# Optimization experiments

Hardware: AMD Instinct MI355X
Metric: run time of the kernel (lower is better)

The kernel has to match this reference:

```python
import jax, jax.numpy as jnp
import numpy as np

H, RANK, BATCH, T = 1024, 4, 128, 256


def setup_inputs() -> dict:
    key = jax.random.key(0)
    ks = jax.random.split(key, 6)
    s = 1.0 / np.sqrt(H)  # glorot-ish scale for params
    return {
        "x": jax.random.normal(ks[0], (BATCH, T, H), jnp.float32),
        "h0": jnp.zeros((BATCH, H), jnp.float32),
        "d": jax.random.normal(ks[1], (H,), jnp.float32) * s,
        "L": jax.random.normal(ks[2], (H, RANK), jnp.float32) * s,
        "R": jax.random.normal(ks[3], (RANK, H), jnp.float32) * s,
        "B": jax.random.normal(ks[4], (H, H), jnp.float32) * s,
    }


def reference(x, h0, d, L, R, B):
    # Input projection B.T @ x_t for all steps at once (one big GEMM):
    # (B.T @ x)_i = sum_j B[j,i] x[j]  ->  x @ B
    xB = jnp.einsum("bth,hk->btk", x, B)  # [batch, T, H]

    def step(h, u):  # h: [batch, H], u: [batch, H]
        # diagonal + rank-4 low-rank update: d*h + L @ (R @ h) + B.T @ x
        low_rank = (h @ R.T) @ L.T  # [batch, H]
        h = jnp.tanh(d * h + low_rank + u)
        return h, h

    _, hs = jax.lax.scan(step, h0, jnp.swapaxes(xB, 0, 1))  # hs: [T, batch, H]
    return jnp.swapaxes(hs, 0, 1)  # [batch, T, H]
```

## Files before the change

### kernel.cpp

```cpp
#include <hip/hip_runtime.h>
#include <hip/hip_bf16.h>

#define H_DIM  1024
#define RANK_  4
#define BATCH_ 128
#define TSTEPS 256
#define M_DIM  (BATCH_ * TSTEPS)

typedef __bf16 bf16x8 __attribute__((ext_vector_type(8)));
typedef float  floatx4 __attribute__((ext_vector_type(4)));
typedef unsigned short ushortx8 __attribute__((ext_vector_type(8)));

__device__ __forceinline__ unsigned short f2bf(float f) {
    unsigned u = __float_as_uint(f);
    u += 0x7FFFu + ((u >> 16) & 1u);
    return (unsigned short)(u >> 16);
}


__global__ __launch_bounds__(256) void cvt_x_kernel(const float* __restrict__ x,
                                                    unsigned short* __restrict__ xb) {
    size_t i = ((size_t)blockIdx.x * 256 + threadIdx.x) * 8;
    float4 v0 = *(const float4*)(x + i);
    float4 v1 = *(const float4*)(x + i + 4);
    ushortx8 o;
    o[0] = f2bf(v0.x); o[1] = f2bf(v0.y); o[2] = f2bf(v0.z); o[3] = f2bf(v0.w);
    o[4] = f2bf(v1.x); o[5] = f2bf(v1.y); o[6] = f2bf(v1.z); o[7] = f2bf(v1.w);
    *(ushortx8*)(xb + i) = o;
}

__global__ __launch_bounds__(256) void cvt_bt_kernel(const float* __restrict__ B,
                                                     unsigned short* __restrict__ Bt) {
    __shared__ float tl[32][33];
    int tx = threadIdx.x & 31, ty = threadIdx.x >> 5;
    int k0 = blockIdx.y * 32, n0 = blockIdx.x * 32;
#pragma unroll
    for (int j = 0; j < 4; ++j)
        tl[ty + 8 * j][tx] = B[(size_t)(k0 + ty + 8 * j) * H_DIM + n0 + tx];
    __syncthreads();
#pragma unroll
    for (int j = 0; j < 4; ++j)
        Bt[(size_t)(n0 + ty + 8 * j) * H_DIM + k0 + tx] = f2bf(tl[tx][ty + 8 * j]);
}


#define TM 128
#define TN 128
#define BK 64

__global__ __launch_bounds__(256) void gemm_bf16_kernel(const unsigned short* __restrict__ A,
                                                        const unsigned short* __restrict__ Bt,
                                                        float* __restrict__ C) {
    __shared__ unsigned short As[TM * BK];
    __shared__ unsigned short Bs[TN * BK];

    const int tid  = threadIdx.x;
    const int lane = tid & 63;
    const int wid  = tid >> 6;
    const int wm = (wid >> 1) * 64, wn = (wid & 1) * 64;
    const int bm = blockIdx.x >> 3, bn = blockIdx.x & 7;
    const int m0 = bm * TM, n0 = bn * TN;

    const int lr = lane & 15;
    const int lk = (lane >> 4) * 8;

    const unsigned short* ag[4];
    const unsigned short* bg[4];
    unsigned short* asl[4];
    unsigned short* bsl[4];
#pragma unroll
    for (int p = 0; p < 4; ++p) {
        const int ab = wid * 4 + p;
        const int rb = ab >> 1, kb = ab & 1;
        ag[p]  = A  + (size_t)(m0 + rb * 16 + lr) * H_DIM + kb * 32 + lk;
        bg[p]  = Bt + (size_t)(n0 + rb * 16 + lr) * H_DIM + kb * 32 + lk;
        asl[p] = As + ab * 512;
        bsl[p] = Bs + ab * 512;
    }

    floatx4 acc[4][4];
#pragma unroll
    for (int i = 0; i < 4; ++i)
#pragma unroll
        for (int j = 0; j < 4; ++j) acc[i][j] = (floatx4){0.f, 0.f, 0.f, 0.f};

    for (int kt = 0; kt < H_DIM; kt += BK) {
        __syncthreads();
#pragma unroll
        for (int p = 0; p < 4; ++p) {
            __builtin_amdgcn_global_load_lds(
                (const __attribute__((address_space(1))) void*)(ag[p] + kt),
                (__attribute__((address_space(3))) void*)asl[p], 16, 0, 0);
            __builtin_amdgcn_global_load_lds(
                (const __attribute__((address_space(1))) void*)(bg[p] + kt),
                (__attribute__((address_space(3))) void*)bsl[p], 16, 0, 0);
        }
        __syncthreads();
#pragma unroll
        for (int kb = 0; kb < 2; ++kb) {
            bf16x8 af[4], bfv[4];
#pragma unroll
            for (int i = 0; i < 4; ++i) {
                const int rbA = (wm >> 4) + i;
                af[i] = *(const bf16x8*)(As + ((rbA * 2 + kb) << 9) + (lane << 3));
            }
#pragma unroll
            for (int j = 0; j < 4; ++j) {
                const int rbB = (wn >> 4) + j;
                bfv[j] = *(const bf16x8*)(Bs + ((rbB * 2 + kb) << 9) + (lane << 3));
            }
#pragma unroll
            for (int i = 0; i < 4; ++i)
#pragma unroll
                for (int j = 0; j < 4; ++j)
                    acc[i][j] = __builtin_amdgcn_mfma_f32_16x16x32_bf16(af[i], bfv[j], acc[i][j], 0, 0, 0);
        }
    }

    const int cr = (lane >> 4) * 4;
    const int cc = lane & 15;
#pragma unroll
    for (int i = 0; i < 4; ++i)
#pragma unroll
        for (int j = 0; j < 4; ++j) {
            size_t base = (size_t)(m0 + wm + i * 16 + cr) * H_DIM + (n0 + wn + j * 16 + cc);
#pragma unroll
            for (int r = 0; r < 4; ++r)
                C[base + (size_t)r * H_DIM] = acc[i][j][r];
        }
}

__global__ __launch_bounds__(256) void gemm_fp32_fallback(const float* __restrict__ A,
                                                          const float* __restrict__ B,
                                                          float* __restrict__ C) {
    __shared__ float As[64][20];
    __shared__ float Bs[16][68];
    const int tid = threadIdx.x;
    const int bm = blockIdx.x >> 4, bn = blockIdx.x & 15;
    const int m0 = bm * 64, n0 = bn * 64;
    const int tx = (tid & 15) * 4, ty = (tid >> 4) * 4;
    float acc[4][4];
#pragma unroll
    for (int i = 0; i < 4; ++i)
#pragma unroll
        for (int j = 0; j < 4; ++j) acc[i][j] = 0.f;

    for (int kk = 0; kk < H_DIM; kk += 16) {
        float4 av = *(const float4*)(A + (size_t)(m0 + (tid >> 2)) * H_DIM + kk + (tid & 3) * 4);
        float4 bv = *(const float4*)(B + (size_t)(kk + (tid >> 4)) * H_DIM + n0 + (tid & 15) * 4);
        __syncthreads();
        *(float4*)&As[tid >> 2][(tid & 3) * 4] = av;
        *(float4*)&Bs[tid >> 4][(tid & 15) * 4] = bv;
        __syncthreads();
#pragma unroll
        for (int k = 0; k < 16; ++k) {
            float a_[4], b_[4];
#pragma unroll
            for (int i = 0; i < 4; ++i) a_[i] = As[ty + i][k];
#pragma unroll
            for (int j = 0; j < 4; ++j) b_[j] = Bs[k][tx + j];
#pragma unroll
            for (int i = 0; i < 4; ++i)
#pragma unroll
                for (int j = 0; j < 4; ++j) acc[i][j] += a_[i] * b_[j];
        }
    }
#pragma unroll
    for (int i = 0; i < 4; ++i)
#pragma unroll
        for (int j = 0; j < 4; ++j)
            C[(size_t)(m0 + ty + i) * H_DIM + n0 + tx + j] = acc[i][j];
}


__device__ __forceinline__ float tanh_fast(float x) {
    float ax = fabsf(x);
    float e  = __expf(-2.0f * ax);
    float t  = (1.0f - e) * __builtin_amdgcn_rcpf(1.0f + e);
    return copysignf(t, x);
}

__device__ __forceinline__ void barrier_lds_only() {
    asm volatile("s_waitcnt lgkmcnt(0)\n\ts_barrier" ::: "memory");
}

template <int CTRL, int RMASK>
__device__ __forceinline__ float dpp_add(float x) {
    int v = __builtin_amdgcn_update_dpp(0, __float_as_int(x), CTRL, RMASK, 0xf, true);
    return x + __int_as_float(v);
}
__device__ __forceinline__ float wave_sum64(float x) {
    x = dpp_add<0x111, 0xf>(x);
    x = dpp_add<0x112, 0xf>(x);
    x = dpp_add<0x114, 0xf>(x);
    x = dpp_add<0x118, 0xf>(x);
    x = dpp_add<0x142, 0xa>(x);
    x = dpp_add<0x143, 0xc>(x);
    return x;
}

__global__ __launch_bounds__(256) void scan_kernel(const float* __restrict__ h0,
                                                   const float* __restrict__ d,
                                                   const float* __restrict__ Lm,
                                                   const float* __restrict__ Rm,
                                                   float* __restrict__ io) {
    const int b = blockIdx.x, tid = threadIdx.x;
    const int lane = tid & 63, wv = tid >> 6;
    const int e = tid * 4;

    float4 dv4 = *(const float4*)(d + e);
    float dd[4] = {dv4.x, dv4.y, dv4.z, dv4.w};
    float4 hv4 = *(const float4*)(h0 + (size_t)b * H_DIM + e);
    float h[4] = {hv4.x, hv4.y, hv4.z, hv4.w};

    float Lv[4][4], Rv[4][4];
#pragma unroll
    for (int i = 0; i < 4; ++i) {
        float4 t = *(const float4*)(Lm + (size_t)(e + i) * RANK_);
        Lv[i][0] = t.x; Lv[i][1] = t.y; Lv[i][2] = t.z; Lv[i][3] = t.w;
    }
#pragma unroll
    for (int j = 0; j < 4; ++j) {
        float4 t = *(const float4*)(Rm + (size_t)j * H_DIM + e);
        Rv[j][0] = t.x; Rv[j][1] = t.y; Rv[j][2] = t.z; Rv[j][3] = t.w;
    }

    float* iob = io + (size_t)b * TSTEPS * H_DIM + e;
    __shared__ float red[2][4][4];

    float4 u[4];
#pragma unroll
    for (int s = 0; s < 4; ++s) u[s] = *(const float4*)(iob + (size_t)s * H_DIM);

    for (int t = 0; t < TSTEPS; t += 4) {
#pragma unroll
        for (int s = 0; s < 4; ++s) {
            const int tt = t + s;
            float pr[4];
#pragma unroll
            for (int j = 0; j < 4; ++j)
                pr[j] = Rv[j][0] * h[0] + Rv[j][1] * h[1] + Rv[j][2] * h[2] + Rv[j][3] * h[3];
#pragma unroll
            for (int j = 0; j < 4; ++j) pr[j] = wave_sum64(pr[j]);
            if (lane == 63) {
                float4 w; w.x = pr[0]; w.y = pr[1]; w.z = pr[2]; w.w = pr[3];
                *(float4*)&red[s & 1][wv][0] = w;
            }
            barrier_lds_only();
            float4 r0 = *(const float4*)&red[s & 1][0][0];
            float4 r1 = *(const float4*)&red[s & 1][1][0];
            float4 r2 = *(const float4*)&red[s & 1][2][0];
            float4 r3 = *(const float4*)&red[s & 1][3][0];
            float r[4] = {r0.x + r1.x + r2.x + r3.x, r0.y + r1.y + r2.y + r3.y,
                          r0.z + r1.z + r2.z + r3.z, r0.w + r1.w + r2.w + r3.w};

            float uu[4] = {u[s].x, u[s].y, u[s].z, u[s].w};
#pragma unroll
            for (int i = 0; i < 4; ++i) {
                float a = fmaf(dd[i], h[i], uu[i]);
                a += Lv[i][0] * r[0] + Lv[i][1] * r[1] + Lv[i][2] * r[2] + Lv[i][3] * r[3];
                h[i] = tanh_fast(a);
            }
            float4 o; o.x = h[0]; o.y = h[1]; o.z = h[2]; o.w = h[3];
            *(float4*)(iob + (size_t)tt * H_DIM) = o;
            if (tt + 4 < TSTEPS) u[s] = *(const float4*)(iob + (size_t)(tt + 4) * H_DIM);
        }
    }
}


extern "C" void kernel_launch(void* const* d_in, const int* in_sizes, int n_in,
                              void* d_out, int out_size, void* d_ws, size_t ws_size,
                              hipStream_t stream) {
    const float* x  = (const float*)d_in[0];
    const float* h0 = (const float*)d_in[1];
    const float* dd = (const float*)d_in[2];
    const float* L  = (const float*)d_in[3];
    const float* R  = (const float*)d_in[4];
    const float* B  = (const float*)d_in[5];
    float* out = (float*)d_out;

    const size_t need = (size_t)M_DIM * H_DIM * sizeof(unsigned short)
                      + (size_t)H_DIM * H_DIM * sizeof(unsigned short);
    if (ws_size >= need) {
        unsigned short* xb = (unsigned short*)d_ws;
        unsigned short* Bt = xb + (size_t)M_DIM * H_DIM;
        cvt_x_kernel<<<(M_DIM * H_DIM) / (256 * 8), 256, 0, stream>>>(x, xb);
        cvt_bt_kernel<<<dim3(32, 32), 256, 0, stream>>>(B, Bt);
        gemm_bf16_kernel<<<(M_DIM / TM) * (H_DIM / TN), 256, 0, stream>>>(xb, Bt, out);
    } else {
        gemm_fp32_fallback<<<(M_DIM / 64) * (H_DIM / 64), 256, 0, stream>>>(x, B, out);
    }
    scan_kernel<<<BATCH_, 256, 0, stream>>>(h0, dd, L, R, out);
}
```

Baseline: 460.9 us.

## Rewrite input-projection GEMM with 256x256 tiles, double-buffered LDS and swizzle

Replaces the 128x128 single-buffered bf16 GEMM with a 256x256-tile, 512-thread kernel. It double-buffers LDS and issues the next tile's global-to-LDS loads in phases interleaved with the MFMA work, coordinated by explicit barriers and waitcnts. It also adds XOR swizzling against LDS bank conflicts, a block-index remap for cache locality, and s_setprio around the MFMA bursts. The aim is to hide global load latency and raise compute density in the GEMM. The cost is more register pressure and fragile hand-tuned synchronisation, while the sequential scan kernel, which likely dominates, is untouched.

```diff
diff --git a/kernel.cpp b/kernel.cpp
--- a/kernel.cpp
+++ b/kernel.cpp
@@ -44,89 +44,133 @@
 }
 
 
-#define TM 128
-#define TN 128
-#define BK 64
-
-__global__ __launch_bounds__(256) void gemm_bf16_kernel(const unsigned short* __restrict__ A,
+#define BM 256
+#define BN 256
+#define BKK 64
+#define KTILES (H_DIM / BKK)
+
+#define GLD(srcptr, dstptr)                                          \
+    __builtin_amdgcn_global_load_lds(                                \
+        (const __attribute__((address_space(1))) void*)(srcptr),     \
+        (__attribute__((address_space(3))) void*)(dstptr), 16, 0, 0)
+
+#define STAGE_A(buf, hf, kt) do {                                                     \
+    GLD(aS0 + (size_t)(hf) * (128 * H_DIM) + (kt) * BKK, &lds[buf][0][hf][dst0]);     \
+    GLD(aS1 + (size_t)(hf) * (128 * H_DIM) + (kt) * BKK, &lds[buf][0][hf][dst1]);     \
+} while (0)
+
+#define STAGE_B(buf, hf, kt) do {                                                     \
+    GLD(bS0 + (size_t)(hf) * (128 * H_DIM) + (kt) * BKK, &lds[buf][1][hf][dst0]);     \
+    GLD(bS1 + (size_t)(hf) * (128 * H_DIM) + (kt) * BKK, &lds[buf][1][hf][dst1]);     \
+} while (0)
+
+#define MFMA_PHASE(q)                                                                                         \
+    _Pragma("unroll")                                                                                         \
+    for (int fc = 0; fc < 4; ++fc) {                                                                          \
+        acc[2*(q)][fc]   = __builtin_amdgcn_mfma_f32_16x16x32_bf16(a00, bfr[fc][0], acc[2*(q)][fc], 0, 0, 0);   \
+        acc[2*(q)][fc]   = __builtin_amdgcn_mfma_f32_16x16x32_bf16(a01, bfr[fc][1], acc[2*(q)][fc], 0, 0, 0);   \
+        acc[2*(q)+1][fc] = __builtin_amdgcn_mfma_f32_16x16x32_bf16(a10, bfr[fc][0], acc[2*(q)+1][fc], 0, 0, 0); \
+        acc[2*(q)+1][fc] = __builtin_amdgcn_mfma_f32_16x16x32_bf16(a11, bfr[fc][1], acc[2*(q)+1][fc], 0, 0, 0); \
+    }
+
+#define PHASE(q, STAGE_STMT, TAIL_STMT) {                                      \
+        bf16x8 a00 = *(const bf16x8*)(Ah + (2*(q))     * 1024 + aRow + cs0);   \
+        bf16x8 a01 = *(const bf16x8*)(Ah + (2*(q))     * 1024 + aRow + cs1);   \
+        bf16x8 a10 = *(const bf16x8*)(Ah + (2*(q) + 1) * 1024 + aRow + cs0);   \
+        bf16x8 a11 = *(const bf16x8*)(Ah + (2*(q) + 1) * 1024 + aRow + cs1);   \
+        STAGE_STMT;                                                            \
+        __builtin_amdgcn_s_barrier();                                          \
+        asm volatile("s_waitcnt lgkmcnt(0)" ::: "memory");                     \
+        __builtin_amdgcn_s_setprio(1);                                         \
+        MFMA_PHASE(q);                                                         \
+        __builtin_amdgcn_s_setprio(0);                                         \
+        TAIL_STMT;                                                             \
+        __builtin_amdgcn_s_barrier();                                          \
+    }
+
+__global__ __launch_bounds__(512, 2) void gemm_bf16_256(const unsigned short* __restrict__ A,
                                                         const unsigned short* __restrict__ Bt,
                                                         float* __restrict__ C) {
-    __shared__ unsigned short As[TM * BK];
-    __shared__ unsigned short Bs[TN * BK];
-
-    const int tid  = threadIdx.x;
-    const int lane = tid & 63;
-    const int wid  = tid >> 6;
-    const int wm = (wid >> 1) * 64, wn = (wid & 1) * 64;
-    const int bm = blockIdx.x >> 3, bn = blockIdx.x & 7;
-    const int m0 = bm * TM, n0 = bn * TN;
-
-    const int lr = lane & 15;
-    const int lk = (lane >> 4) * 8;
-
-    const unsigned short* ag[4];
-    const unsigned short* bg[4];
-    unsigned short* asl[4];
-    unsigned short* bsl[4];
-#pragma unroll
-    for (int p = 0; p < 4; ++p) {
-        const int ab = wid * 4 + p;
-        const int rb = ab >> 1, kb = ab & 1;
-        ag[p]  = A  + (size_t)(m0 + rb * 16 + lr) * H_DIM + kb * 32 + lk;
-        bg[p]  = Bt + (size_t)(n0 + rb * 16 + lr) * H_DIM + kb * 32 + lk;
-        asl[p] = As + ab * 512;
-        bsl[p] = Bs + ab * 512;
-    }
-
-    floatx4 acc[4][4];
-#pragma unroll
-    for (int i = 0; i < 4; ++i)
+    __shared__ unsigned short lds[2][2][2][8192];
+
+    const int tid = threadIdx.x;
+    const int l   = tid & 63;
+    const int w   = tid >> 6;
+    const int wr  = w >> 2;
+    const int wc  = w & 3;
+
+    const int bid = blockIdx.x;
+    const int lt  = (bid & 7) * 64 + (bid >> 3);
+    const int m0  = (lt >> 2) * BM;
+    const int n0  = (lt & 3)  * BN;
+
+    const int p0row = (w * 2 + 0) * 8 + (l >> 3);
+    const int p1row = (w * 2 + 1) * 8 + (l >> 3);
+    const int gcol  = ((l & 7) ^ (l >> 3)) * 8;
+    const int dst0  = (w * 2 + 0) * 512;
+    const int dst1  = (w * 2 + 1) * 512;
+    const unsigned short* aS0 = A  + (size_t)(m0 + p0row) * H_DIM + gcol;
+    const unsigned short* aS1 = A  + (size_t)(m0 + p1row) * H_DIM + gcol;
+    const unsigned short* bS0 = Bt + (size_t)(n0 + p0row) * H_DIM + gcol;
+    const unsigned short* bS1 = Bt + (size_t)(n0 + p1row) * H_DIM + gcol;
+
+    const int aRow = (l & 15) * 64;
+    const int cs0  = (((l >> 4) + 0) ^ (l & 7)) * 8;
+    const int cs1  = (((l >> 4) + 4) ^ (l & 7)) * 8;
+
+    floatx4 acc[8][4];
+#pragma unroll
+    for (int i = 0; i < 8; ++i)
 #pragma unroll
         for (int j = 0; j < 4; ++j) acc[i][j] = (floatx4){0.f, 0.f, 0.f, 0.f};
 
-    for (int kt = 0; kt < H_DIM; kt += BK) {
-        __syncthreads();
-#pragma unroll
-        for (int p = 0; p < 4; ++p) {
-            __builtin_amdgcn_global_load_lds(
-                (const __attribute__((address_space(1))) void*)(ag[p] + kt),
-                (__attribute__((address_space(3))) void*)asl[p], 16, 0, 0);
-            __builtin_amdgcn_global_load_lds(
-                (const __attribute__((address_space(1))) void*)(bg[p] + kt),
-                (__attribute__((address_space(3))) void*)bsl[p], 16, 0, 0);
+    STAGE_B(0, 0, 0); STAGE_B(0, 1, 0); STAGE_A(0, 0, 0); STAGE_A(0, 1, 0);
+    STAGE_B(1, 0, 1); STAGE_B(1, 1, 1); STAGE_A(1, 0, 1);
+    asm volatile("s_waitcnt vmcnt(6)" ::: "memory");
+    __builtin_amdgcn_s_barrier();
+
+    for (int kt = 0; kt < KTILES; ++kt) {
+        const int buf = kt & 1;
+        const unsigned short* Ah = &lds[buf][0][wr][0];
+        const unsigned short* Bh = &lds[buf][1][wc >> 1][(wc & 1) * 4096];
+        bf16x8 bfr[4][2];
+
+        {
+            bf16x8 a00 = *(const bf16x8*)(Ah + 0 * 1024 + aRow + cs0);
+            bf16x8 a01 = *(const bf16x8*)(Ah + 0 * 1024 + aRow + cs1);
+            bf16x8 a10 = *(const bf16x8*)(Ah + 1 * 1024 + aRow + cs0);
+            bf16x8 a11 = *(const bf16x8*)(Ah + 1 * 1024 + aRow + cs1);
+#pragma unroll
+            for (int fc = 0; fc < 4; ++fc) {
+                bfr[fc][0] = *(const bf16x8*)(Bh + fc * 1024 + aRow + cs0);
+                bfr[fc][1] = *(const bf16x8*)(Bh + fc * 1024 + aRow + cs1);
+            }
+            if (kt + 1 < KTILES) STAGE_A(buf ^ 1, 1, kt + 1);
+            __builtin_amdgcn_s_barrier();
+            asm volatile("s_waitcnt lgkmcnt(0)" ::: "memory");
+            __builtin_amdgcn_s_setprio(1);
+            MFMA_PHASE(0);
+            __builtin_amdgcn_s_setprio(0);
+            __builtin_amdgcn_s_barrier();
         }
-        __syncthreads();
-#pragma unroll
-        for (int kb = 0; kb < 2; ++kb) {
-            bf16x8 af[4], bfv[4];
-#pragma unroll
-            for (int i = 0; i < 4; ++i) {
-                const int rbA = (wm >> 4) + i;
-                af[i] = *(const bf16x8*)(As + ((rbA * 2 + kb) << 9) + (lane << 3));
-            }
-#pragma unroll
-            for (int j = 0; j < 4; ++j) {
-                const int rbB = (wn >> 4) + j;
-                bfv[j] = *(const bf16x8*)(Bs + ((rbB * 2 + kb) << 9) + (lane << 3));
-            }
-#pragma unroll
-            for (int i = 0; i < 4; ++i)
-#pragma unroll
-                for (int j = 0; j < 4; ++j)
-                    acc[i][j] = __builtin_amdgcn_mfma_f32_16x16x32_bf16(af[i], bfv[j], acc[i][j], 0, 0, 0);
-        }
-    }
-
-    const int cr = (lane >> 4) * 4;
-    const int cc = lane & 15;
-#pragma unroll
-    for (int i = 0; i < 4; ++i)
-#pragma unroll
-        for (int j = 0; j < 4; ++j) {
-            size_t base = (size_t)(m0 + wm + i * 16 + cr) * H_DIM + (n0 + wn + j * 16 + cc);
+        PHASE(1, if (kt + 2 < KTILES) STAGE_B(buf, 0, kt + 2), );
+        PHASE(2, if (kt + 2 < KTILES) STAGE_B(buf, 1, kt + 2), );
+        PHASE(3, if (kt + 2 < KTILES) STAGE_A(buf, 0, kt + 2),
+              if (kt < KTILES - 2) { asm volatile("s_waitcnt vmcnt(6)" ::: "memory"); }
+              else if (kt == KTILES - 2) { asm volatile("s_waitcnt vmcnt(0)" ::: "memory"); });
+    }
+
+    const int cr = (l >> 4) * 4;
+    const int cc = l & 15;
+#pragma unroll
+    for (int fr = 0; fr < 8; ++fr)
+#pragma unroll
+        for (int fc = 0; fc < 4; ++fc) {
+            size_t base = (size_t)(m0 + wr * 128 + fr * 16 + cr) * H_DIM
+                        + (n0 + wc * 64 + fc * 16 + cc);
 #pragma unroll
             for (int r = 0; r < 4; ++r)
-                C[base + (size_t)r * H_DIM] = acc[i][j][r];
+                C[base + (size_t)r * H_DIM] = acc[fr][fc][r];
         }
 }
 
@@ -287,7 +331,7 @@
         unsigned short* Bt = xb + (size_t)M_DIM * H_DIM;
         cvt_x_kernel<<<(M_DIM * H_DIM) / (256 * 8), 256, 0, stream>>>(x, xb);
         cvt_bt_kernel<<<dim3(32, 32), 256, 0, stream>>>(B, Bt);
-        gemm_bf16_kernel<<<(M_DIM / TM) * (H_DIM / TN), 256, 0, stream>>>(xb, Bt, out);
+        gemm_bf16_256<<<(M_DIM / BM) * (H_DIM / BN), 512, 0, stream>>>(xb, Bt, out);
     } else {
         gemm_fp32_fallback<<<(M_DIM / 64) * (H_DIM / 64), 256, 0, stream>>>(x, B, out);
     }
```

Result: faster. 395.5 us (-14.2%).
